# Performance work log

Measured on AMD Instinct MI355X. Metric: run time of the kernel, lower is better.

## Reference

```python
import jax, jax.numpy as jnp
from jax import lax
import numpy as np

B, M, C, H, W = 32, 2, 256, 16, 16
N = H * W            # 256, square case required by the original bmm chain
DIM = 256            # hardcoded self.dim in the module
THR = 0.1
RATIO = 0.8


def conv2d(x, w, b):
    y = lax.conv_general_dilated(x, w, (1, 1), 'SAME',
                                 dimension_numbers=('NCHW', 'OIHW', 'NCHW'))
    return y + b[None, :, None, None]


def setup_inputs() -> dict:
    key = jax.random.key(0)
    ks = jax.random.split(key, 8)
    return {
        'con_feat': jax.random.normal(ks[0], (B, M, C, H, W), jnp.float32),
        'feat_s':   jax.random.normal(ks[1], (B, M, C, C), jnp.float32),
        'feat_v':   jax.random.uniform(ks[2], (B, M, C), jnp.float32),
        'feat_d':   jax.random.normal(ks[3], (B, M, N, N), jnp.float32),
        'w_enc':    jax.random.normal(ks[4], (C, C, 3, 3), jnp.float32) * 0.02,
        'b_enc':    jnp.zeros((C,), jnp.float32),
        'w_dec':    jax.random.normal(ks[5], (C, C, 3, 3), jnp.float32) * 0.02,
        'b_dec':    jnp.zeros((C,), jnp.float32),
        'w_val':    jax.random.normal(ks[6], (1, 2 * C, 3, 3), jnp.float32) * 0.02,
        'b_val':    jnp.zeros((1,), jnp.float32),
    }


def _assemble(fs, fv, fd, counts):
    # fs: (M,C,C) row blocks, fv: (M,C) diag values, fd: (M,N,N) col blocks, counts: (M,)
    big = max(C, N)                                  # out-of-range sentinel -> dropped
    off = jnp.cumsum(counts) - counts                # exclusive prefix offsets (M,)
    r = jnp.arange(C)
    dest = off[:, None] + r[None, :]                 # (M,C) destination slots
    valid = (r[None, :] < counts[:, None]) & (dest >= 0)
    dest = jnp.where(valid, dest, big).reshape(-1)   # (M*C,)
    ns = jnp.zeros((C, C), fs.dtype).at[dest].set(fs.reshape(M * C, C), mode='drop')
    fd_cols = fd[:, :, :C].transpose(0, 2, 1).reshape(M * C, N)  # source columns as rows
    ndT = jnp.zeros((N, N), fd.dtype).at[dest].set(fd_cols, mode='drop')
    nv = jnp.zeros((C, N), fv.dtype).at[dest, dest].set(fv.reshape(-1), mode='drop')
    return ns, nv, ndT.T


def reference(con_feat, feat_s, feat_v, feat_d, w_enc, b_enc, w_dec, b_dec, w_val, b_val):
    x = con_feat.reshape(B * M, C, H, W)
    # autoencoder reconstruction loss (training branch)
    mid = jax.nn.relu(conv2d(x, w_enc, b_enc))
    x_rec = conv2d(mid, w_dec, b_dec)
    auto_enc_loss = jnp.mean((x - x_rec) ** 2)

    # data-dependent rank budget per (batch, modality)
    counts = jnp.sum(feat_v > THR, axis=-1).astype(jnp.int32)      # (B,M)
    total = jnp.sum(counts, axis=-1)                               # (B,)
    kmin = min(C, N)
    adj = jnp.round(kmin * counts.astype(jnp.float32)
                    / jnp.maximum(total, 1)[:, None].astype(jnp.float32)).astype(jnp.int32)
    if M > 1:
        adj = adj.at[:, -1].set(DIM - jnp.sum(adj[:, :-1], axis=-1))
    counts = jnp.maximum(jnp.where((total > kmin)[:, None], adj, counts), 0)

    # scatter-assemble s/v/d and reconstruct
    ns, nv, nd = jax.vmap(_assemble)(feat_s, feat_v, feat_d, counts)
    rec = jnp.matmul(jnp.matmul(ns, nv), nd)                        # (B,C,N)
    rec = rec.reshape(B, C, H, W)
    rec = conv2d(rec, w_dec, b_dec)                                 # decoder
    rec = (rec - rec.min()) / (rec.max() - rec.min()) * 2.0 - 1.0

    # per-modality value scores, softmax over modality
    scores = jnp.stack([
        jax.nn.sigmoid(jax.nn.relu(conv2d(
            jnp.concatenate([rec, con_feat[:, m]], axis=1), w_val, b_val)))
        for m in range(M)
    ], axis=1)                                                      # (B,M,1,H,W)
    scores = jax.nn.softmax(scores, axis=1)
    fused = jnp.sum((1.0 - RATIO) * scores * con_feat, axis=1) + rec * RATIO
    return fused, auto_enc_loss
```

## Files before the change

### kernel.cpp

```cpp
#include <hip/hip_runtime.h>
#include <math.h>


typedef __attribute__((ext_vector_type(8))) short short8;
typedef __attribute__((ext_vector_type(4))) float f32x4;

__device__ __forceinline__ void gload_lds16(const void* g, void* l) {
  __builtin_amdgcn_global_load_lds(
      (const __attribute__((address_space(1))) void*)g,
      (__attribute__((address_space(3))) void*)l, 16, 0, 0);
}

__device__ __forceinline__ unsigned short f2bf(float f) {
  unsigned u = __float_as_uint(f);
  unsigned r = (u + 0x7FFFu + ((u >> 16) & 1u)) >> 16;
  return (unsigned short)r;
}

__device__ __forceinline__ unsigned mapf(float f) {
  unsigned u = __float_as_uint(f);
  return (u & 0x80000000u) ? ~u : (u | 0x80000000u);
}
__device__ __forceinline__ float unmapf(unsigned u) {
  unsigned v = (u & 0x80000000u) ? (u & 0x7fffffffu) : ~u;
  return __uint_as_float(v);
}

__global__ __launch_bounds__(256) void prep_k(
    const float* __restrict__ cf, const float* __restrict__ we,
    const float* __restrict__ wd, const float* __restrict__ fv,
    unsigned short* __restrict__ Xp, unsigned short* __restrict__ WrE,
    unsigned short* __restrict__ WrD, int* __restrict__ smr,
    float* __restrict__ vd, float4* __restrict__ sraw4,
    float* __restrict__ lacc, unsigned* __restrict__ mm) {
  const int bx = blockIdx.x, t = threadIdx.x;
  if (bx < 2048) {
    int idx = bx * 256 + t;
    int ch = idx & 31, p = (idx >> 5) & 255, img = idx >> 13;
    int ic0 = ch * 8;
    const float* sp = cf + (size_t)img * 65536 + (size_t)ic0 * 256 + p;
    unsigned short h[8];
#pragma unroll
    for (int i = 0; i < 8; ++i) h[i] = f2bf(sp[i * 256]);
    int y = p >> 4, x = p & 15;
    uint4 u;
    u.x = h[0] | (h[1] << 16); u.y = h[2] | (h[3] << 16);
    u.z = h[4] | (h[5] << 16); u.w = h[6] | (h[7] << 16);
    *(uint4*)&Xp[(size_t)img * 82944 + (size_t)(y * 18 + x + 19) * 256 + ic0] = u;
  } else if (bx < 2624) {
    int idx = (bx - 2048) * 256 + t;
    int ch = idx & 31, rest = idx >> 5;
    int s = rest % 9, ocx = rest / 9;
    int oc = ocx & 255, cv = ocx >> 8;
    const float* w = cv ? wd : we;
    unsigned short* o = cv ? WrD : WrE;
    int ic0 = ch * 8;
    unsigned short h[8];
#pragma unroll
    for (int i = 0; i < 8; ++i) h[i] = f2bf(w[(size_t)oc * 2304 + (ic0 + i) * 9 + s]);
    uint4 u;
    u.x = h[0] | (h[1] << 16); u.y = h[2] | (h[3] << 16);
    u.z = h[4] | (h[5] << 16); u.w = h[6] | (h[7] << 16);
    *(uint4*)&o[(size_t)oc * 2304 + s * 256 + ic0] = u;
  } else if (bx < 2752) {
    int img = bx - 2624;
    uint4* base = (uint4*)Xp + (size_t)img * 10368;
    uint4 z; z.x = z.y = z.z = z.w = 0;
    for (int it = t; it < 2176; it += 256) {
      int px = it >> 5, c = it & 31;
      int y, x;
      if (px < 18)      { y = 0;  x = px; }
      else if (px < 36) { y = 17; x = px - 18; }
      else if (px < 52) { y = px - 35; x = 0; }
      else              { y = px - 51; x = 17; }
      base[(y * 18 + x) * 32 + c] = z;
    }
  } else if (bx < 2784) {
    const int b = bx - 2752;
    const float v0 = fv[(size_t)b * 512 + t];
    const float v1 = fv[(size_t)b * 512 + 256 + t];
    const unsigned long long bal0 = __ballot(v0 > 0.1f);
    const unsigned long long bal1 = __ballot(v1 > 0.1f);
    __shared__ int cnt0[4], cnt1[4], fc[2];
    const int wid = t >> 6, lane = t & 63;
    if (lane == 0) { cnt0[wid] = __popcll(bal0); cnt1[wid] = __popcll(bal1); }
    smr[b * 256 + t] = -1;
    vd[b * 256 + t] = 0.f;
    __syncthreads();
    if (t == 0) {
      int c0 = cnt0[0] + cnt0[1] + cnt0[2] + cnt0[3];
      int c1 = cnt1[0] + cnt1[1] + cnt1[2] + cnt1[3];
      int total = c0 + c1;
      int f0, f1;
      if (total > 256) {
        int a0 = (int)rintf(256.0f * (float)c0 / (float)total);
        f0 = a0; f1 = 256 - a0;
      } else { f0 = c0; f1 = c1; }
      fc[0] = max(f0, 0); fc[1] = max(f1, 0);
    }
    __syncthreads();
    const int c0 = fc[0], c1 = fc[1];
    if (t < c0) { smr[b * 256 + t] = t; vd[b * 256 + t] = v0; }
    if (t < c1) {
      int d = c0 + t;
      if (d < 256) { smr[b * 256 + d] = 256 + t; vd[b * 256 + d] = v1; }
    }
  } else {
    int z = bx - 2784;
    if (z < 24) {
      float4 zz; zz.x = zz.y = zz.z = zz.w = 0.f;
      sraw4[z * 256 + t] = zz;
    } else if (t == 0) {
      lacc[0] = 0.f; mm[0] = 0xFFFFFFFFu; mm[1] = 0u;
    }
  }
}

template<int EPI>
__global__ __launch_bounds__(256) void convmma_k(
    const unsigned short* __restrict__ Xin, const unsigned short* __restrict__ Wr,
    const float* __restrict__ bias, const float* __restrict__ cfref,
    unsigned short* __restrict__ outp, float* __restrict__ outf,
    float* __restrict__ lacc, unsigned* __restrict__ mm) {
  __shared__ __align__(16) unsigned short As[8192];
  __shared__ __align__(16) unsigned short Bs[16384];
  const int t = threadIdx.x, lane = t & 63, wave = t >> 6;
  const int img = blockIdx.y, pt = blockIdx.x >> 1, ot = blockIdx.x & 1;

  int laneA[4], laneB[8];
  {
    const int rl = lane >> 4, lc = lane & 15;
#pragma unroll
    for (int j = 0; j < 4; ++j) {
      int row = (wave * 4 + j) * 4 + rl;
      int p = pt * 64 + row;
      int y = p >> 4, x = p & 15;
      laneA[j] = (y * 18 + x) * 512 + ((lc ^ (row & 15)) * 16);
    }
#pragma unroll
    for (int j = 0; j < 8; ++j) {
      int row = (wave * 8 + j) * 4 + rl;
      laneB[j] = (ot * 128 + row) * 4608 + ((lc ^ (row & 15)) * 16);
    }
  }
  const char* Ag = (const char*)Xin + (size_t)img * 165888;
  const char* Bg = (const char*)Wr;

  const int mlane = lane & 15, quad = lane >> 4;
  const int mw = wave >> 1, nw = wave & 1;
  int aoff[2][4], boff[4][4];
#pragma unroll
  for (int ks = 0; ks < 4; ++ks) {
#pragma unroll
    for (int i = 0; i < 2; ++i) {
      int rowm = mw * 32 + i * 16 + mlane;
      aoff[i][ks] = rowm * 256 + (((ks * 4 + quad) ^ (rowm & 15)) * 16);
    }
#pragma unroll
    for (int n = 0; n < 4; ++n) {
      int rown = nw * 64 + n * 16 + mlane;
      boff[n][ks] = rown * 256 + (((ks * 4 + quad) ^ (rown & 15)) * 16);
    }
  }

  f32x4 acc[2][4] = {};

  for (int kit = 0; kit < 18; ++kit) {
    int s = kit >> 1, kc = kit & 1;
    int dy = s / 3, dx = s - dy * 3;
    int aG = (dy * 18 + dx) * 512 + kc * 256;
    int bG = kit << 8;
    __syncthreads();
#pragma unroll
    for (int j = 0; j < 4; ++j)
      gload_lds16(Ag + laneA[j] + aG, (char*)As + (wave * 4 + j) * 1024);
#pragma unroll
    for (int j = 0; j < 8; ++j)
      gload_lds16(Bg + laneB[j] + bG, (char*)Bs + (wave * 8 + j) * 1024);
    __syncthreads();
#pragma unroll
    for (int ks = 0; ks < 4; ++ks) {
      short8 af[2], bf[4];
#pragma unroll
      for (int i = 0; i < 2; ++i)
        af[i] = *(const short8*)((const char*)As + aoff[i][ks]);
#pragma unroll
      for (int n = 0; n < 4; ++n)
        bf[n] = *(const short8*)((const char*)Bs + boff[n][ks]);
#pragma unroll
      for (int i = 0; i < 2; ++i)
#pragma unroll
        for (int n = 0; n < 4; ++n)
          acc[i][n] = __builtin_amdgcn_mfma_f32_16x16x32_bf16(af[i], bf[n], acc[i][n], 0, 0, 0);
    }
  }

  if (EPI == 0) {
#pragma unroll
    for (int i = 0; i < 2; ++i) {
      int m0 = pt * 64 + mw * 32 + i * 16 + quad * 4;
#pragma unroll
      for (int n = 0; n < 4; ++n) {
        int oc = ot * 128 + nw * 64 + n * 16 + mlane;
        float bv = bias[oc];
#pragma unroll
        for (int r = 0; r < 4; ++r) {
          int p = m0 + r;
          int y = p >> 4, x = p & 15;
          float v = fmaxf(acc[i][n][r] + bv, 0.f);
          outp[(size_t)img * 82944 + (size_t)(y * 18 + x + 19) * 256 + oc] = f2bf(v);
        }
      }
    }
  } else if (EPI == 1) {
    float ls = 0.f;
#pragma unroll
    for (int i = 0; i < 2; ++i) {
      int m0 = pt * 64 + mw * 32 + i * 16 + quad * 4;
#pragma unroll
      for (int n = 0; n < 4; ++n) {
        int oc = ot * 128 + nw * 64 + n * 16 + mlane;
        float bv = bias[oc];
        float4 c4 = *(const float4*)(cfref + (size_t)img * 65536 + (size_t)oc * 256 + m0);
        float d0 = acc[i][n][0] + bv - c4.x;
        float d1 = acc[i][n][1] + bv - c4.y;
        float d2 = acc[i][n][2] + bv - c4.z;
        float d3 = acc[i][n][3] + bv - c4.w;
        ls += d0 * d0 + d1 * d1 + d2 * d2 + d3 * d3;
      }
    }
#pragma unroll
    for (int off = 32; off; off >>= 1) ls += __shfl_down(ls, off);
    __shared__ float sred[4];
    if (lane == 0) sred[wave] = ls;
    __syncthreads();
    if (t == 0) atomicAdd(lacc, sred[0] + sred[1] + sred[2] + sred[3]);
  } else {
    float mn = INFINITY, mx = -INFINITY;
#pragma unroll
    for (int i = 0; i < 2; ++i) {
      int m0 = pt * 64 + mw * 32 + i * 16 + quad * 4;
#pragma unroll
      for (int n = 0; n < 4; ++n) {
        int oc = ot * 128 + nw * 64 + n * 16 + mlane;
        float bv = bias[oc];
        float4 v;
        v.x = acc[i][n][0] + bv; v.y = acc[i][n][1] + bv;
        v.z = acc[i][n][2] + bv; v.w = acc[i][n][3] + bv;
        mn = fminf(mn, fminf(fminf(v.x, v.y), fminf(v.z, v.w)));
        mx = fmaxf(mx, fmaxf(fmaxf(v.x, v.y), fmaxf(v.z, v.w)));
        *(float4*)(outf + (size_t)img * 65536 + (size_t)oc * 256 + m0) = v;
      }
    }
#pragma unroll
    for (int off = 32; off; off >>= 1) {
      mn = fminf(mn, __shfl_down(mn, off));
      mx = fmaxf(mx, __shfl_down(mx, off));
    }
    __shared__ float smn[4], smx[4];
    if (lane == 0) { smn[wave] = mn; smx[wave] = mx; }
    __syncthreads();
    if (t == 0) {
      mn = fminf(fminf(smn[0], smn[1]), fminf(smn[2], smn[3]));
      mx = fmaxf(fmaxf(smx[0], smx[1]), fmaxf(smx[2], smx[3]));
      atomicMin(&mm[0], mapf(mn));
      atomicMax(&mm[1], mapf(mx));
    }
  }
}

__global__ __launch_bounds__(256) void ansbmt_k(
    const float* __restrict__ fs, const float* __restrict__ fd,
    const int* __restrict__ smr, const float* __restrict__ vd,
    unsigned short* __restrict__ Ans, unsigned short* __restrict__ BmT,
    unsigned short* __restrict__ Recp) {
  const int bx = blockIdx.x, t = threadIdx.x;
  if (bx < 1024) {
    int idx = bx * 256 + t;
    int ch = idx & 31, c = (idx >> 5) & 255, b = idx >> 13;
    int j0 = ch * 8;
    int si = smr[b * 256 + c];
    unsigned short h[8] = {0, 0, 0, 0, 0, 0, 0, 0};
    if (si >= 0) {
      int m = si >> 8, r = si & 255;
      const float* fp = fs + (((size_t)b * 2 + m) * 256 + r) * 256 + j0;
      const float* vp = vd + b * 256 + j0;
#pragma unroll
      for (int i = 0; i < 8; ++i) h[i] = f2bf(fp[i] * vp[i]);
    }
    uint4 u;
    u.x = h[0] | (h[1] << 16); u.y = h[2] | (h[3] << 16);
    u.z = h[4] | (h[5] << 16); u.w = h[6] | (h[7] << 16);
    *(uint4*)&Ans[(size_t)b * 65536 + c * 256 + j0] = u;
  } else if (bx < 1152) {
    __shared__ float sIn[4096];
    const int b = (bx - 1024) >> 2, bz = (bx - 1024) & 3;
    const int sp = smr[b * 256 + t];
    const int m_p = sp >> 8, r_p = sp & 255;
    for (int jg = bz * 8; jg < bz * 8 + 8; ++jg) {
      __syncthreads();
#pragma unroll
      for (int u = 0; u < 4; ++u) {
        int q = t * 4 + u;
        int rr = q >> 6, w = q & 63;
        int m = rr >> 3, i = rr & 7;
        float4 f = ((const float4*)fd)[((size_t)(b * 2 + m) * 256 + jg * 8 + i) * 64 + w];
        *(float4*)&sIn[i * 512 + m * 256 + w * 4] = f;
      }
      __syncthreads();
      unsigned short h[8] = {0, 0, 0, 0, 0, 0, 0, 0};
      if (sp >= 0) {
#pragma unroll
        for (int i = 0; i < 8; ++i) h[i] = f2bf(sIn[i * 512 + m_p * 256 + r_p]);
      }
      uint4 u;
      u.x = h[0] | (h[1] << 16); u.y = h[2] | (h[3] << 16);
      u.z = h[4] | (h[5] << 16); u.w = h[6] | (h[7] << 16);
      *(uint4*)&BmT[(size_t)b * 65536 + t * 256 + jg * 8] = u;
    }
  } else {
    int img = bx - 1152;
    uint4* base = (uint4*)Recp + (size_t)img * 10368;
    uint4 z; z.x = z.y = z.z = z.w = 0;
    for (int it = t; it < 2176; it += 256) {
      int px = it >> 5, c = it & 31;
      int y, x;
      if (px < 18)      { y = 0;  x = px; }
      else if (px < 36) { y = 17; x = px - 18; }
      else if (px < 52) { y = px - 35; x = 0; }
      else              { y = px - 51; x = 17; }
      base[(y * 18 + x) * 32 + c] = z;
    }
  }
}

__global__ __launch_bounds__(256) void recgemm_k(const unsigned short* __restrict__ BmT,
                                                 const unsigned short* __restrict__ Ans,
                                                 unsigned short* __restrict__ Recp) {
  __shared__ __align__(16) unsigned short As[8192];
  __shared__ __align__(16) unsigned short Bs[16384];
  const int t = threadIdx.x, lane = t & 63, wave = t >> 6;
  const int b = blockIdx.y, pt = blockIdx.x >> 1, ct = blockIdx.x & 1;

  int laneA[4], laneB[8];
  {
    const int rl = lane >> 4, lc = lane & 15;
#pragma unroll
    for (int j = 0; j < 4; ++j) {
      int row = (wave * 4 + j) * 4 + rl;
      laneA[j] = (pt * 64 + row) * 512 + ((lc ^ (row & 15)) * 16);
    }
#pragma unroll
    for (int j = 0; j < 8; ++j) {
      int row = (wave * 8 + j) * 4 + rl;
      laneB[j] = (ct * 128 + row) * 512 + ((lc ^ (row & 15)) * 16);
    }
  }
  const char* Ag = (const char*)BmT + (size_t)b * 131072;
  const char* Bg = (const char*)Ans + (size_t)b * 131072;

  const int mlane = lane & 15, quad = lane >> 4;
  const int mw = wave >> 1, nw = wave & 1;
  int aoff[2][4], boff[4][4];
#pragma unroll
  for (int ks = 0; ks < 4; ++ks) {
#pragma unroll
    for (int i = 0; i < 2; ++i) {
      int rowm = mw * 32 + i * 16 + mlane;
      aoff[i][ks] = rowm * 256 + (((ks * 4 + quad) ^ (rowm & 15)) * 16);
    }
#pragma unroll
    for (int n = 0; n < 4; ++n) {
      int rown = nw * 64 + n * 16 + mlane;
      boff[n][ks] = rown * 256 + (((ks * 4 + quad) ^ (rown & 15)) * 16);
    }
  }

  f32x4 acc[2][4] = {};

  for (int kit = 0; kit < 2; ++kit) {
    int g = kit << 8;
    __syncthreads();
#pragma unroll
    for (int j = 0; j < 4; ++j)
      gload_lds16(Ag + laneA[j] + g, (char*)As + (wave * 4 + j) * 1024);
#pragma unroll
    for (int j = 0; j < 8; ++j)
      gload_lds16(Bg + laneB[j] + g, (char*)Bs + (wave * 8 + j) * 1024);
    __syncthreads();
#pragma unroll
    for (int ks = 0; ks < 4; ++ks) {
      short8 af[2], bf[4];
#pragma unroll
      for (int i = 0; i < 2; ++i)
        af[i] = *(const short8*)((const char*)As + aoff[i][ks]);
#pragma unroll
      for (int n = 0; n < 4; ++n)
        bf[n] = *(const short8*)((const char*)Bs + boff[n][ks]);
#pragma unroll
      for (int i = 0; i < 2; ++i)
#pragma unroll
        for (int n = 0; n < 4; ++n)
          acc[i][n] = __builtin_amdgcn_mfma_f32_16x16x32_bf16(af[i], bf[n], acc[i][n], 0, 0, 0);
    }
  }

#pragma unroll
  for (int i = 0; i < 2; ++i) {
    int m0 = pt * 64 + mw * 32 + i * 16 + quad * 4;
#pragma unroll
    for (int n = 0; n < 4; ++n) {
      int cc = ct * 128 + nw * 64 + n * 16 + mlane;
#pragma unroll
      for (int r = 0; r < 4; ++r) {
        int p = m0 + r;
        int y = p >> 4, x = p & 15;
        Recp[(size_t)b * 82944 + (size_t)(y * 18 + x + 19) * 256 + cc] = f2bf(acc[i][n][r]);
      }
    }
  }
}

__global__ __launch_bounds__(256) void score_conv_k(
    const float* __restrict__ rec2, const float* __restrict__ cf,
    const float* __restrict__ wval, const unsigned* __restrict__ mm,
    float* __restrict__ sraw) {
  const int b = blockIdx.x, phase = blockIdx.y, icc = blockIdx.z;
  const int t = threadIdx.x;
  const int row = t >> 4, col = t & 15;
  __shared__ float s_in[8 * 360];
  __shared__ float s_wv[72];
  for (int i = t; i < 8 * 360; i += 256) s_in[i] = 0.f;
  const float* src;
  float sc = 1.f, sh = 0.f;
  int wofs;
  if (phase == 0) {
    src = rec2 + (size_t)b * 65536;
    float mn = unmapf(mm[0]), mx = unmapf(mm[1]);
    sc = 2.f / (mx - mn);
    sh = -mn * sc - 1.f;
    wofs = 0;
  } else {
    src = cf + ((size_t)b * 2 + (phase - 1)) * 65536;
    wofs = 2304;
  }
  float acc = 0.f;
  for (int ic0 = icc * 64; ic0 < icc * 64 + 64; ic0 += 8) {
    __syncthreads();
#pragma unroll
    for (int i = 0; i < 8; ++i) {
      float v = src[(ic0 + i) * 256 + t];
      if (phase == 0) v = fmaf(v, sc, sh);
      s_in[i * 360 + (row + 1) * 20 + (col + 1)] = v;
    }
    if (t < 72) s_wv[t] = wval[wofs + ic0 * 9 + t];
    __syncthreads();
#pragma unroll
    for (int i = 0; i < 8; ++i)
#pragma unroll
      for (int ky = 0; ky < 3; ++ky)
#pragma unroll
        for (int kx = 0; kx < 3; ++kx)
          acc += s_in[i * 360 + (row + ky) * 20 + (col + kx)] * s_wv[i * 9 + ky * 3 + kx];
  }
  atomicAdd(&sraw[((size_t)b * 3 + phase) * 256 + t], acc);
}

__global__ void fuse_k(const float* __restrict__ cf, const float* __restrict__ rec2,
                       const float* __restrict__ sraw, const float* __restrict__ bval,
                       const unsigned* __restrict__ mm, const float* __restrict__ lacc,
                       float* __restrict__ outp) {
  const int idx = blockIdx.x * 256 + threadIdx.x;
  const int b = idx >> 16;
  const int rest = idx & 65535;
  const int pos = idx & 255;
  const float mn = unmapf(mm[0]), mx = unmapf(mm[1]);
  const float sc = 2.f / (mx - mn), sh = -mn * sc - 1.f;
  const float srec = sraw[(size_t)b * 768 + pos];
  const float sc0 = sraw[(size_t)b * 768 + 256 + pos];
  const float sc1 = sraw[(size_t)b * 768 + 512 + pos];
  const float bv = bval[0];
  const float z0 = fmaxf(srec + sc0 + bv, 0.f);
  const float z1 = fmaxf(srec + sc1 + bv, 0.f);
  const float s0 = 1.f / (1.f + expf(-z0));
  const float s1 = 1.f / (1.f + expf(-z1));
  const float w0 = 1.f / (1.f + expf(s1 - s0));
  const float w1 = 1.f - w0;
  const float rn = fmaf(rec2[idx], sc, sh);
  const float f0 = cf[(size_t)b * 131072 + rest];
  const float f1 = cf[(size_t)b * 131072 + 65536 + rest];
  outp[idx] = 0.2f * (w0 * f0 + w1 * f1) + 0.8f * rn;
  if (idx == 0) outp[2097152] = lacc[0] * (1.f / 4194304.f);
}

extern "C" void kernel_launch(void* const* d_in, const int* in_sizes, int n_in,
                              void* d_out, int out_size, void* d_ws, size_t ws_size,
                              hipStream_t stream) {
  const float* cf    = (const float*)d_in[0];
  const float* fs    = (const float*)d_in[1];
  const float* fv    = (const float*)d_in[2];
  const float* fd    = (const float*)d_in[3];
  const float* w_enc = (const float*)d_in[4];
  const float* b_enc = (const float*)d_in[5];
  const float* w_dec = (const float*)d_in[6];
  const float* b_dec = (const float*)d_in[7];
  const float* w_val = (const float*)d_in[8];
  const float* b_val = (const float*)d_in[9];
  float* out = (float*)d_out;
  float* wsf = (float*)d_ws;

  unsigned short* Xp   = (unsigned short*)wsf;
  unsigned short* Ans  = (unsigned short*)wsf;
  unsigned short* BmT  = (unsigned short*)(wsf + 1048576);
  unsigned short* Midp = (unsigned short*)(wsf + 2654208);
  unsigned short* Recp = (unsigned short*)(wsf + 2654208);
  float* rec2 = wsf + 5308416;
  unsigned short* WrE = (unsigned short*)(wsf + 7405568);
  unsigned short* WrD = (unsigned short*)(wsf + 7700480);
  float* sraw = wsf + 7995392;
  float* vd   = wsf + 8019968;
  int*   smr  = (int*)(wsf + 8028160);
  float* lacc = wsf + 8036352;
  unsigned* mm = (unsigned*)(wsf + 8036354);

  prep_k<<<2809, 256, 0, stream>>>(cf, w_enc, w_dec, fv, Xp, WrE, WrD, smr, vd,
                                   (float4*)sraw, lacc, mm);
  convmma_k<0><<<dim3(8, 64), 256, 0, stream>>>(Xp, WrE, b_enc, nullptr, Midp, nullptr, nullptr, nullptr);
  convmma_k<1><<<dim3(8, 64), 256, 0, stream>>>(Midp, WrD, b_dec, cf, nullptr, nullptr, lacc, nullptr);
  ansbmt_k<<<1184, 256, 0, stream>>>(fs, fd, smr, vd, Ans, BmT, Recp);
  recgemm_k<<<dim3(8, 32), 256, 0, stream>>>(BmT, Ans, Recp);
  convmma_k<2><<<dim3(8, 32), 256, 0, stream>>>(Recp, WrD, b_dec, nullptr, nullptr, rec2, nullptr, mm);
  score_conv_k<<<dim3(32, 3, 4), 256, 0, stream>>>(rec2, cf, w_val, mm, sraw);
  fuse_k<<<8192, 256, 0, stream>>>(cf, rec2, sraw, b_val, mm, lacc, out);
}
```

Baseline: 253.0 us.

## Double-buffer conv and rec GEMMs with smaller tiles and more blocks

The implicit-GEMM conv kernels and the reconstruction GEMM now use 64x64 output tiles with a 64-wide K step, and a two-stage LDS double buffer. The next stage's global-to-LDS loads are issued before computing on the current buffer, replacing the two-barrier load-then-compute loop. Grids double, and the score conv is split over 8 channel chunks instead of 4. The aim is more blocks in flight and load latency hidden behind MFMA work. The cost is less reuse per tile, more global traffic, and more atomics.

After: 265.4 us. 4.9% more time.

```diff
diff --git a/kernel.cpp b/kernel.cpp
--- a/kernel.cpp
+++ b/kernel.cpp
@@ -117,80 +117,75 @@
 }
 
 template<int EPI>
-__global__ __launch_bounds__(256) void convmma_k(
+__global__ __launch_bounds__(256, 4) void convmma_k(
     const unsigned short* __restrict__ Xin, const unsigned short* __restrict__ Wr,
     const float* __restrict__ bias, const float* __restrict__ cfref,
     unsigned short* __restrict__ outp, float* __restrict__ outf,
     float* __restrict__ lacc, unsigned* __restrict__ mm) {
-  __shared__ __align__(16) unsigned short As[8192];
-  __shared__ __align__(16) unsigned short Bs[16384];
+  __shared__ __align__(16) unsigned short S[2][8192];
   const int t = threadIdx.x, lane = t & 63, wave = t >> 6;
-  const int img = blockIdx.y, pt = blockIdx.x >> 1, ot = blockIdx.x & 1;
-
-  int laneA[4], laneB[8];
-  {
-    const int rl = lane >> 4, lc = lane & 15;
-#pragma unroll
-    for (int j = 0; j < 4; ++j) {
-      int row = (wave * 4 + j) * 4 + rl;
-      int p = pt * 64 + row;
-      int y = p >> 4, x = p & 15;
-      laneA[j] = (y * 18 + x) * 512 + ((lc ^ (row & 15)) * 16);
-    }
-#pragma unroll
-    for (int j = 0; j < 8; ++j) {
-      int row = (wave * 8 + j) * 4 + rl;
-      laneB[j] = (ot * 128 + row) * 4608 + ((lc ^ (row & 15)) * 16);
-    }
+  const int img = blockIdx.y, pt = blockIdx.x >> 2, ot = blockIdx.x & 3;
+
+  int laneA[2], laneB[2];
+#pragma unroll
+  for (int j = 0; j < 2; ++j) {
+    int id = (wave * 2 + j) * 64 + lane;
+    int row = id >> 3, q = (id & 7) ^ (row & 7);
+    int p = pt * 64 + row, y = p >> 4, x = p & 15;
+    laneA[j] = (y * 18 + x) * 512 + q * 16;
+    laneB[j] = (ot * 64 + row) * 4608 + q * 16;
   }
   const char* Ag = (const char*)Xin + (size_t)img * 165888;
   const char* Bg = (const char*)Wr;
 
   const int mlane = lane & 15, quad = lane >> 4;
   const int mw = wave >> 1, nw = wave & 1;
-  int aoff[2][4], boff[4][4];
-#pragma unroll
-  for (int ks = 0; ks < 4; ++ks) {
+  int aoff[2][2], boff[2][2];
+#pragma unroll
+  for (int ks = 0; ks < 2; ++ks) {
 #pragma unroll
     for (int i = 0; i < 2; ++i) {
       int rowm = mw * 32 + i * 16 + mlane;
-      aoff[i][ks] = rowm * 256 + (((ks * 4 + quad) ^ (rowm & 15)) * 16);
-    }
-#pragma unroll
-    for (int n = 0; n < 4; ++n) {
-      int rown = nw * 64 + n * 16 + mlane;
-      boff[n][ks] = rown * 256 + (((ks * 4 + quad) ^ (rown & 15)) * 16);
-    }
-  }
-
-  f32x4 acc[2][4] = {};
-
-  for (int kit = 0; kit < 18; ++kit) {
-    int s = kit >> 1, kc = kit & 1;
+      aoff[i][ks] = rowm * 128 + (((ks * 4 + quad) ^ (rowm & 7)) * 16);
+      int rown = nw * 32 + i * 16 + mlane;
+      boff[i][ks] = 8192 + rown * 128 + (((ks * 4 + quad) ^ (rown & 7)) * 16);
+    }
+  }
+
+  auto stage = [&](int kit, int buf) {
+    int s = kit >> 2;
     int dy = s / 3, dx = s - dy * 3;
-    int aG = (dy * 18 + dx) * 512 + kc * 256;
-    int bG = kit << 8;
-    __syncthreads();
-#pragma unroll
-    for (int j = 0; j < 4; ++j)
-      gload_lds16(Ag + laneA[j] + aG, (char*)As + (wave * 4 + j) * 1024);
-#pragma unroll
-    for (int j = 0; j < 8; ++j)
-      gload_lds16(Bg + laneB[j] + bG, (char*)Bs + (wave * 8 + j) * 1024);
-    __syncthreads();
-#pragma unroll
-    for (int ks = 0; ks < 4; ++ks) {
-      short8 af[2], bf[4];
+    int aG = (dy * 18 + dx) * 512 + (kit & 3) * 128;
+    int bG = kit * 128;
+    char* dst = (char*)S[buf];
+#pragma unroll
+    for (int j = 0; j < 2; ++j)
+      gload_lds16(Ag + laneA[j] + aG, dst + (wave * 2 + j) * 1024);
+#pragma unroll
+    for (int j = 0; j < 2; ++j)
+      gload_lds16(Bg + laneB[j] + bG, dst + 8192 + (wave * 2 + j) * 1024);
+  };
+
+  f32x4 acc[2][2] = {};
+  stage(0, 0);
+  for (int kit = 0; kit < 36; ++kit) {
+    int cur = kit & 1;
+    asm volatile("s_waitcnt vmcnt(0)" ::: "memory");
+    asm volatile("s_barrier" ::: "memory");
+    if (kit + 1 < 36) stage(kit + 1, 1 - cur);
+    const char* Sb = (const char*)S[cur];
+#pragma unroll
+    for (int ks = 0; ks < 2; ++ks) {
+      short8 af[2], bf[2];
+#pragma unroll
+      for (int i = 0; i < 2; ++i) {
+        af[i] = *(const short8*)(Sb + aoff[i][ks]);
+        bf[i] = *(const short8*)(Sb + boff[i][ks]);
+      }
 #pragma unroll
       for (int i = 0; i < 2; ++i)
-        af[i] = *(const short8*)((const char*)As + aoff[i][ks]);
-#pragma unroll
-      for (int n = 0; n < 4; ++n)
-        bf[n] = *(const short8*)((const char*)Bs + boff[n][ks]);
-#pragma unroll
-      for (int i = 0; i < 2; ++i)
-#pragma unroll
-        for (int n = 0; n < 4; ++n)
+#pragma unroll
+        for (int n = 0; n < 2; ++n)
           acc[i][n] = __builtin_amdgcn_mfma_f32_16x16x32_bf16(af[i], bf[n], acc[i][n], 0, 0, 0);
     }
   }
@@ -200,8 +195,8 @@
     for (int i = 0; i < 2; ++i) {
       int m0 = pt * 64 + mw * 32 + i * 16 + quad * 4;
 #pragma unroll
-      for (int n = 0; n < 4; ++n) {
-        int oc = ot * 128 + nw * 64 + n * 16 + mlane;
+      for (int n = 0; n < 2; ++n) {
+        int oc = ot * 64 + nw * 32 + n * 16 + mlane;
         float bv = bias[oc];
 #pragma unroll
         for (int r = 0; r < 4; ++r) {
@@ -218,8 +213,8 @@
     for (int i = 0; i < 2; ++i) {
       int m0 = pt * 64 + mw * 32 + i * 16 + quad * 4;
 #pragma unroll
-      for (int n = 0; n < 4; ++n) {
-        int oc = ot * 128 + nw * 64 + n * 16 + mlane;
+      for (int n = 0; n < 2; ++n) {
+        int oc = ot * 64 + nw * 32 + n * 16 + mlane;
         float bv = bias[oc];
         float4 c4 = *(const float4*)(cfref + (size_t)img * 65536 + (size_t)oc * 256 + m0);
         float d0 = acc[i][n][0] + bv - c4.x;
@@ -241,8 +236,8 @@
     for (int i = 0; i < 2; ++i) {
       int m0 = pt * 64 + mw * 32 + i * 16 + quad * 4;
 #pragma unroll
-      for (int n = 0; n < 4; ++n) {
-        int oc = ot * 128 + nw * 64 + n * 16 + mlane;
+      for (int n = 0; n < 2; ++n) {
+        int oc = ot * 64 + nw * 32 + n * 16 + mlane;
         float bv = bias[oc];
         float4 v;
         v.x = acc[i][n][0] + bv; v.y = acc[i][n][1] + bv;
@@ -334,73 +329,69 @@
   }
 }
 
-__global__ __launch_bounds__(256) void recgemm_k(const unsigned short* __restrict__ BmT,
-                                                 const unsigned short* __restrict__ Ans,
-                                                 unsigned short* __restrict__ Recp) {
-  __shared__ __align__(16) unsigned short As[8192];
-  __shared__ __align__(16) unsigned short Bs[16384];
+__global__ __launch_bounds__(256, 4) void recgemm_k(const unsigned short* __restrict__ BmT,
+                                                    const unsigned short* __restrict__ Ans,
+                                                    unsigned short* __restrict__ Recp) {
+  __shared__ __align__(16) unsigned short S[2][8192];
   const int t = threadIdx.x, lane = t & 63, wave = t >> 6;
-  const int b = blockIdx.y, pt = blockIdx.x >> 1, ct = blockIdx.x & 1;
-
-  int laneA[4], laneB[8];
-  {
-    const int rl = lane >> 4, lc = lane & 15;
-#pragma unroll
-    for (int j = 0; j < 4; ++j) {
-      int row = (wave * 4 + j) * 4 + rl;
-      laneA[j] = (pt * 64 + row) * 512 + ((lc ^ (row & 15)) * 16);
-    }
-#pragma unroll
-    for (int j = 0; j < 8; ++j) {
-      int row = (wave * 8 + j) * 4 + rl;
-      laneB[j] = (ct * 128 + row) * 512 + ((lc ^ (row & 15)) * 16);
-    }
+  const int b = blockIdx.y, pt = blockIdx.x >> 2, ct = blockIdx.x & 3;
+
+  int laneA[2], laneB[2];
+#pragma unroll
+  for (int j = 0; j < 2; ++j) {
+    int id = (wave * 2 + j) * 64 + lane;
+    int row = id >> 3, q = (id & 7) ^ (row & 7);
+    laneA[j] = (pt * 64 + row) * 512 + q * 16;
+    laneB[j] = (ct * 64 + row) * 512 + q * 16;
   }
   const char* Ag = (const char*)BmT + (size_t)b * 131072;
   const char* Bg = (const char*)Ans + (size_t)b * 131072;
 
   const int mlane = lane & 15, quad = lane >> 4;
   const int mw = wave >> 1, nw = wave & 1;
-  int aoff[2][4], boff[4][4];
-#pragma unroll
-  for (int ks = 0; ks < 4; ++ks) {
+  int aoff[2][2], boff[2][2];
+#pragma unroll
+  for (int ks = 0; ks < 2; ++ks) {
 #pragma unroll
     for (int i = 0; i < 2; ++i) {
       int rowm = mw * 32 + i * 16 + mlane;
-      aoff[i][ks] = rowm * 256 + (((ks * 4 + quad) ^ (rowm & 15)) * 16);
-    }
-#pragma unroll
-    for (int n = 0; n < 4; ++n) {
-      int rown = nw * 64 + n * 16 + mlane;
-      boff[n][ks] = rown * 256 + (((ks * 4 + quad) ^ (rown & 15)) * 16);
-    }
-  }
-
-  f32x4 acc[2][4] = {};
-
-  for (int kit = 0; kit < 2; ++kit) {
-    int g = kit << 8;
-    __syncthreads();
-#pragma unroll
-    for (int j = 0; j < 4; ++j)
-      gload_lds16(Ag + laneA[j] + g, (char*)As + (wave * 4 + j) * 1024);
-#pragma unroll
-    for (int j = 0; j < 8; ++j)
-      gload_lds16(Bg + laneB[j] + g, (char*)Bs + (wave * 8 + j) * 1024);
-    __syncthreads();
-#pragma unroll
-    for (int ks = 0; ks < 4; ++ks) {
-      short8 af[2], bf[4];
+      aoff[i][ks] = rowm * 128 + (((ks * 4 + quad) ^ (rowm & 7)) * 16);
+      int rown = nw * 32 + i * 16 + mlane;
+      boff[i][ks] = 8192 + rown * 128 + (((ks * 4 + quad) ^ (rown & 7)) * 16);
+    }
+  }
+
+  auto stage = [&](int kit, int buf) {
+    int g = kit * 128;
+    char* dst = (char*)S[buf];
+#pragma unroll
+    for (int j = 0; j < 2; ++j)
+      gload_lds16(Ag + laneA[j] + g, dst + (wave * 2 + j) * 1024);
+#pragma unroll
+    for (int j = 0; j < 2; ++j)
+      gload_lds16(Bg + laneB[j] + g, dst + 8192 + (wave * 2 + j) * 1024);
+  };
+
+  f32x4 acc[2][2] = {};
+  stage(0, 0);
+  for (int kit = 0; kit < 4; ++kit) {
+    int cur = kit & 1;
+    asm volatile("s_waitcnt vmcnt(0)" ::: "memory");
+    asm volatile("s_barrier" ::: "memory");
+    if (kit + 1 < 4) stage(kit + 1, 1 - cur);
+    const char* Sb = (const char*)S[cur];
+#pragma unroll
+    for (int ks = 0; ks < 2; ++ks) {
+      short8 af[2], bf[2];
+#pragma unroll
+      for (int i = 0; i < 2; ++i) {
+        af[i] = *(const short8*)(Sb + aoff[i][ks]);
+        bf[i] = *(const short8*)(Sb + boff[i][ks]);
+      }
 #pragma unroll
       for (int i = 0; i < 2; ++i)
-        af[i] = *(const short8*)((const char*)As + aoff[i][ks]);
-#pragma unroll
-      for (int n = 0; n < 4; ++n)
-        bf[n] = *(const short8*)((const char*)Bs + boff[n][ks]);
-#pragma unroll
-      for (int i = 0; i < 2; ++i)
-#pragma unroll
-        for (int n = 0; n < 4; ++n)
+#pragma unroll
+        for (int n = 0; n < 2; ++n)
           acc[i][n] = __builtin_amdgcn_mfma_f32_16x16x32_bf16(af[i], bf[n], acc[i][n], 0, 0, 0);
     }
   }
@@ -409,8 +400,8 @@
   for (int i = 0; i < 2; ++i) {
     int m0 = pt * 64 + mw * 32 + i * 16 + quad * 4;
 #pragma unroll
-    for (int n = 0; n < 4; ++n) {
-      int cc = ct * 128 + nw * 64 + n * 16 + mlane;
+    for (int n = 0; n < 2; ++n) {
+      int cc = ct * 64 + nw * 32 + n * 16 + mlane;
 #pragma unroll
       for (int r = 0; r < 4; ++r) {
         int p = m0 + r;
@@ -445,7 +436,7 @@
     wofs = 2304;
   }
   float acc = 0.f;
-  for (int ic0 = icc * 64; ic0 < icc * 64 + 64; ic0 += 8) {
+  for (int ic0 = icc * 32; ic0 < icc * 32 + 32; ic0 += 8) {
     __syncthreads();
 #pragma unroll
     for (int i = 0; i < 8; ++i) {
@@ -525,11 +516,11 @@
 
   prep_k<<<2809, 256, 0, stream>>>(cf, w_enc, w_dec, fv, Xp, WrE, WrD, smr, vd,
                                    (float4*)sraw, lacc, mm);
-  convmma_k<0><<<dim3(8, 64), 256, 0, stream>>>(Xp, WrE, b_enc, nullptr, Midp, nullptr, nullptr, nullptr);
-  convmma_k<1><<<dim3(8, 64), 256, 0, stream>>>(Midp, WrD, b_dec, cf, nullptr, nullptr, lacc, nullptr);
+  convmma_k<0><<<dim3(16, 64), 256, 0, stream>>>(Xp, WrE, b_enc, nullptr, Midp, nullptr, nullptr, nullptr);
+  convmma_k<1><<<dim3(16, 64), 256, 0, stream>>>(Midp, WrD, b_dec, cf, nullptr, nullptr, lacc, nullptr);
   ansbmt_k<<<1184, 256, 0, stream>>>(fs, fd, smr, vd, Ans, BmT, Recp);
-  recgemm_k<<<dim3(8, 32), 256, 0, stream>>>(BmT, Ans, Recp);
-  convmma_k<2><<<dim3(8, 32), 256, 0, stream>>>(Recp, WrD, b_dec, nullptr, nullptr, rec2, nullptr, mm);
-  score_conv_k<<<dim3(32, 3, 4), 256, 0, stream>>>(rec2, cf, w_val, mm, sraw);
+  recgemm_k<<<dim3(16, 32), 256, 0, stream>>>(BmT, Ans, Recp);
+  convmma_k<2><<<dim3(16, 32), 256, 0, stream>>>(Recp, WrD, b_dec, nullptr, nullptr, rec2, nullptr, mm);
+  score_conv_k<<<dim3(32, 3, 8), 256, 0, stream>>>(rec2, cf, w_val, mm, sraw);
   fuse_k<<<8192, 256, 0, stream>>>(cf, rec2, sraw, b_val, mm, lacc, out);
 }
```
